# Optimization experiments

Measured on AMD Instinct MI355X. Metric: run time of the kernel, lower is better.

## Reference

```python
import jax, jax.numpy as jnp
import numpy as np

# static config (matches init_kwargs)
B, H, W, C = 8, 64, 64, 512
HEADS, WS, SHIFT = 16, 8, 4
N = WS * WS
HIDDEN = 4 * C
HEAD_DIM = C // HEADS
SCALE = HEAD_DIM ** -0.5
EPS = 1e-3  # keras LayerNormalization default epsilon


def _rel_pos_index(ws):
    # replicates tf.meshgrid default 'xy' indexing used in the source
    coords = np.stack(np.meshgrid(np.arange(ws), np.arange(ws)))  # [2, ws, ws]
    cf = coords.reshape(2, -1)
    rel = (cf[:, :, None] - cf[:, None, :]).transpose(1, 2, 0)  # [N, N, 2]
    rel[:, :, 0] += ws - 1
    rel[:, :, 1] += ws - 1
    rel[:, :, 0] *= 2 * ws - 1
    return jnp.asarray(rel.sum(-1))  # [N, N] int


def _attn_mask(h, w, ws, shift):
    img = np.zeros((h, w), dtype=np.float32)
    cnt = 0
    for hs in (slice(0, -ws), slice(-ws, -shift), slice(-shift, None)):
        for wsl in (slice(0, -ws), slice(-ws, -shift), slice(-shift, None)):
            img[hs, wsl] = cnt
            cnt += 1
    mw = img.reshape(h // ws, ws, w // ws, ws).transpose(0, 2, 1, 3).reshape(-1, ws * ws)  # [nW, N]
    diff = mw[:, None, :] - mw[:, :, None]
    return jnp.asarray(np.where(diff != 0, -100.0, 0.0).astype(np.float32))  # [nW, N, N]


REL_IDX = _rel_pos_index(WS)
ATTN_MASK = _attn_mask(H, W, WS, SHIFT)
NW = (H // WS) * (W // WS)


def _ln(x, g, b):
    mu = jnp.mean(x, -1, keepdims=True)
    var = jnp.mean(jnp.square(x - mu), -1, keepdims=True)
    return (x - mu) * jax.lax.rsqrt(var + EPS) * g + b


def setup_inputs() -> dict:
    key = jax.random.key(0)
    ks = jax.random.split(key, 14)
    s = 0.02
    return {
        "x": jax.random.normal(ks[0], (B, H * W, C), jnp.float32),
        "norm1_g": jnp.ones((C,), jnp.float32),
        "norm1_b": jnp.zeros((C,), jnp.float32),
        "qkv_w": jax.random.normal(ks[1], (C, 3 * C), jnp.float32) * s,
        "qkv_b": jnp.zeros((3 * C,), jnp.float32),
        "rpb_table": jax.random.normal(ks[2], ((2 * WS - 1) ** 2, HEADS), jnp.float32) * s,
        "proj_w": jax.random.normal(ks[3], (C, C), jnp.float32) * s,
        "proj_b": jnp.zeros((C,), jnp.float32),
        "norm2_g": jnp.ones((C,), jnp.float32),
        "norm2_b": jnp.zeros((C,), jnp.float32),
        "fc1_w": jax.random.normal(ks[4], (C, HIDDEN), jnp.float32) * s,
        "fc1_b": jnp.zeros((HIDDEN,), jnp.float32),
        "fc2_w": jax.random.normal(ks[5], (HIDDEN, C), jnp.float32) * s,
        "fc2_b": jnp.zeros((C,), jnp.float32),
    }


def reference(x, norm1_g, norm1_b, qkv_w, qkv_b, rpb_table, proj_w, proj_b,
              norm2_g, norm2_b, fc1_w, fc1_b, fc2_w, fc2_b):
    shortcut = x
    h = _ln(x, norm1_g, norm1_b).reshape(B, H, W, C)
    # cyclic shift (SW-MSA)
    h = jnp.roll(h, (-SHIFT, -SHIFT), axis=(1, 2))
    # window partition -> (B*nW, N, C)
    h = h.reshape(B, H // WS, WS, W // WS, WS, C).transpose(0, 1, 3, 2, 4, 5)
    h = h.reshape(B * NW, N, C)
    # qkv
    qkv = (h @ qkv_w + qkv_b).reshape(B * NW, N, 3, HEADS, HEAD_DIM).transpose(2, 0, 3, 1, 4)
    q, k, v = qkv[0] * SCALE, qkv[1], qkv[2]  # each [Bw, heads, N, hd]
    attn = jnp.einsum('bhnd,bhmd->bhnm', q, k)  # [Bw, heads, N, N]
    bias = rpb_table[REL_IDX.reshape(-1)].reshape(N, N, HEADS).transpose(2, 0, 1)
    attn = attn + bias[None]
    # shifted-window mask, per source: mask add -> softmax -> softmax AGAIN (source quirk)
    attn = attn.reshape(B, NW, HEADS, N, N) + ATTN_MASK[None, :, None]
    attn = attn.reshape(B * NW, HEADS, N, N)
    attn = jax.nn.softmax(attn, axis=-1)
    attn = jax.nn.softmax(attn, axis=-1)
    o = jnp.einsum('bhnm,bhmd->bhnd', attn, v).transpose(0, 2, 1, 3).reshape(B * NW, N, C)
    o = o @ proj_w + proj_b
    # window reverse + reverse shift
    o = o.reshape(B, H // WS, W // WS, WS, WS, C).transpose(0, 1, 3, 2, 4, 5).reshape(B, H, W, C)
    o = jnp.roll(o, (SHIFT, SHIFT), axis=(1, 2)).reshape(B, H * W, C)
    x = shortcut + o
    # MLP: source applies gelu twice (Dense activation + explicit gelu)
    y = _ln(x, norm2_g, norm2_b)
    y = jax.nn.gelu(jax.nn.gelu(y @ fc1_w + fc1_b, approximate=False), approximate=False)
    y = y @ fc2_w + fc2_b
    return x + y
```

## Files before the change

### kernel.cpp

```cpp
#include <hip/hip_runtime.h>
#include <hip/hip_bf16.h>
#include <math.h>


typedef unsigned short ushort_t;
typedef __attribute__((ext_vector_type(8))) short short8;
typedef __attribute__((ext_vector_type(8))) __bf16 bf16x8;
typedef __attribute__((ext_vector_type(4))) float f32x4;

#define DEVINL __device__ __forceinline__

union frag_u { short8 s; bf16x8 b; };

DEVINL float bf2f(ushort_t u){ union {unsigned int i; float f;} c; c.i = ((unsigned)u)<<16; return c.f; }
DEVINL ushort_t f2bf(float f){ union {unsigned int i; float f;} c; c.f = f; unsigned r = c.i + 0x7fffu + ((c.i>>16)&1u); return (ushort_t)(r>>16); }

typedef const __attribute__((address_space(1))) void* gas_t;
typedef __attribute__((address_space(3))) void* las_t;
DEVINL void load_lds16(const void* g, void* l) {
  __builtin_amdgcn_global_load_lds((gas_t)g, (las_t)l, 16, 0, 0);
}

DEVINL float gelu_fast(float v){
  float z  = fabsf(v) * 0.70710678118654752f;
  float t  = __builtin_amdgcn_rcpf(fmaf(0.47047f, z, 1.0f));
  float p  = t * fmaf(t, fmaf(t, 0.7478556f, -0.0958798f), 0.3480242f);
  float e  = __expf(-z*z);
  float er = fmaf(-p, e, 1.0f);
  float hs = (v >= 0.f) ? 0.5f : -0.5f;
  return v * fmaf(hs, er, 0.5f);
}

DEVINL int win_map_row(int t){
  int bw = t >> 6, n = t & 63;
  int b  = bw >> 6, wdx = bw & 63;
  int wh = wdx >> 3, ww = wdx & 7;
  int r  = n >> 3,  c  = n & 7;
  int hh = (wh*8 + r + 4) & 63;
  int w2 = (ww*8 + c + 4) & 63;
  return (b << 12) + (hh << 6) + w2;
}

__global__ void transpose_f2b(const float* __restrict__ in, ushort_t* __restrict__ out,
                              int R, int Ccols){
  __shared__ float t[32][33];
  int bx = blockIdx.x*32, by = blockIdx.y*32;
  int x = threadIdx.x, y = threadIdx.y;
  #pragma unroll
  for (int i=0;i<32;i+=8) t[y+i][x] = in[(size_t)(by+y+i)*Ccols + bx + x];
  __syncthreads();
  #pragma unroll
  for (int i=0;i<32;i+=8) out[(size_t)(bx+y+i)*R + by + x] = f2bf(t[x][y+i]);
}

__global__ __launch_bounds__(256) void ln_kernel(const float* __restrict__ in,
    const float* __restrict__ g, const float* __restrict__ bta,
    ushort_t* __restrict__ out, int windowed){
  int tid = threadIdx.x; int l = tid & 63; int w = tid >> 6;
  int t = blockIdx.x * 4 + w;
  int src = windowed ? win_map_row(t) : t;
  const float* row = in + (size_t)src * 512;
  float4 v0 = *(const float4*)(row + l*8);
  float4 v1 = *(const float4*)(row + l*8 + 4);
  float f[8] = {v0.x,v0.y,v0.z,v0.w, v1.x,v1.y,v1.z,v1.w};
  float s=0.f, s2=0.f;
  #pragma unroll
  for (int j=0;j<8;j++){ s += f[j]; s2 += f[j]*f[j]; }
  #pragma unroll
  for (int m=1;m<64;m<<=1){ s += __shfl_xor(s,m); s2 += __shfl_xor(s2,m); }
  float mu  = s * (1.f/512.f);
  float var = s2*(1.f/512.f) - mu*mu;
  float rs  = rsqrtf(var + 1e-3f);
  float4 g0 = *(const float4*)(g + l*8),   g1 = *(const float4*)(g + l*8 + 4);
  float4 b0 = *(const float4*)(bta + l*8), b1 = *(const float4*)(bta + l*8 + 4);
  float gg[8] = {g0.x,g0.y,g0.z,g0.w, g1.x,g1.y,g1.z,g1.w};
  float bb[8] = {b0.x,b0.y,b0.z,b0.w, b1.x,b1.y,b1.z,b1.w};
  short8 o;
  #pragma unroll
  for (int j=0;j<8;j++) o[j] = (short)f2bf((f[j]-mu)*rs*gg[j] + bb[j]);
  *(short8*)(out + (size_t)t*512 + l*8) = o;
}

#define G_STAGE(G, base, h, tt, LB) do { \
    load_lds16((G) + (base) + (size_t)((h)*128)*K    + (size_t)(tt)*64, &lds[(LB) + (h)*8192 +        w*512]); \
    load_lds16((G) + (base) + (size_t)((h)*128+64)*K + (size_t)(tt)*64, &lds[(LB) + (h)*8192 + 4096 + w*512]); \
  } while(0)

#define NOWAIT
#define VM4 asm volatile("s_waitcnt vmcnt(4)" ::: "memory")

#define PHASE(mp, STAGE_STMT, EXTRA) do { \
    bf16x8 a0 = *(const bf16x8*)&lds[ALb + aoff[2*(mp)  ][0]]; \
    bf16x8 a1 = *(const bf16x8*)&lds[ALb + aoff[2*(mp)  ][1]]; \
    bf16x8 a2 = *(const bf16x8*)&lds[ALb + aoff[2*(mp)+1][0]]; \
    bf16x8 a3 = *(const bf16x8*)&lds[ALb + aoff[2*(mp)+1][1]]; \
    STAGE_STMT; \
    EXTRA; \
    __builtin_amdgcn_s_barrier(); \
    asm volatile("s_waitcnt lgkmcnt(0)" ::: "memory"); \
    __builtin_amdgcn_sched_barrier(0); \
    __builtin_amdgcn_s_setprio(1); \
    _Pragma("unroll") \
    for (int nf=0; nf<4; nf++){ \
      acc[2*(mp)  ][nf] = __builtin_amdgcn_mfma_f32_16x16x32_bf16(a0, bfr[nf][0], acc[2*(mp)  ][nf], 0,0,0); \
      acc[2*(mp)  ][nf] = __builtin_amdgcn_mfma_f32_16x16x32_bf16(a1, bfr[nf][1], acc[2*(mp)  ][nf], 0,0,0); \
      acc[2*(mp)+1][nf] = __builtin_amdgcn_mfma_f32_16x16x32_bf16(a2, bfr[nf][0], acc[2*(mp)+1][nf], 0,0,0); \
      acc[2*(mp)+1][nf] = __builtin_amdgcn_mfma_f32_16x16x32_bf16(a3, bfr[nf][1], acc[2*(mp)+1][nf], 0,0,0); \
    } \
    __builtin_amdgcn_s_setprio(0); \
    __builtin_amdgcn_sched_barrier(0); \
    __builtin_amdgcn_s_barrier(); \
  } while(0)

template<int EPI>
__global__ __launch_bounds__(512, 2) void gemm256(
    const ushort_t* __restrict__ A, const ushort_t* __restrict__ Bt,
    const float* __restrict__ bias, void* __restrict__ Cout_v,
    const float* __restrict__ xres, int M, int N, int K)
{
  __shared__ ushort_t lds[65536];
  const int tid = threadIdx.x; const int l = tid & 63; const int w = tid >> 6;
  const int wm = w >> 2, wn = w & 3;
  const int m0 = blockIdx.x*256, n0 = blockIdx.y*256;
  const int lr = l & 15, lk = l >> 4;
  const int nt = K >> 6;

  const int r0 = tid >> 3;
  const int kc = ((tid & 7) - r0) & 7;
  const size_t aRow0 = (size_t)(m0 + r0) * K + kc * 8;
  const size_t bRow0 = (size_t)(n0 + r0) * K + kc * 8;

  int aoff[8][2], boff[4][2];
  #pragma unroll
  for (int mf=0; mf<8; mf++){
    int row = wm*128 + mf*16 + lr;
    #pragma unroll
    for (int kh=0; kh<2; kh++){ int c = kh*4 + lk; aoff[mf][kh] = (row*8 + ((c + row)&7))*8; }
  }
  #pragma unroll
  for (int nf=0; nf<4; nf++){
    int row = wn*64 + nf*16 + lr;
    #pragma unroll
    for (int kh=0; kh<2; kh++){ int c = kh*4 + lk; boff[nf][kh] = (row*8 + ((c + row)&7))*8; }
  }

  f32x4 acc[8][4] = {};

  G_STAGE(A,  aRow0, 0, 0, 0);
  G_STAGE(A,  aRow0, 1, 0, 0);
  G_STAGE(Bt, bRow0, 0, 0, 16384);
  G_STAGE(Bt, bRow0, 1, 0, 16384);
  G_STAGE(Bt, bRow0, 0, 1, 32768+16384);
  G_STAGE(Bt, bRow0, 1, 1, 32768+16384);
  VM4;
  __builtin_amdgcn_s_barrier();

  #pragma unroll 2
  for (int t = 0; t < nt; ++t) {
    const int b   = t & 1;
    const int ALb = b*32768, BLb = ALb + 16384;
    const int ALn = (b^1)*32768;
    const int t1  = (t+1 < nt) ? t+1 : t;
    const int t2  = (t+2 < nt) ? t+2 : t;

    bf16x8 bfr[4][2];
    #pragma unroll
    for (int nf=0; nf<4; nf++){
      bfr[nf][0] = *(const bf16x8*)&lds[BLb + boff[nf][0]];
      bfr[nf][1] = *(const bf16x8*)&lds[BLb + boff[nf][1]];
    }
    PHASE(0, G_STAGE(A,  aRow0, 0, t1, ALn), NOWAIT);
    PHASE(1, G_STAGE(A,  aRow0, 1, t1, ALn), NOWAIT);
    PHASE(2, G_STAGE(Bt, bRow0, 0, t2, BLb), NOWAIT);
    PHASE(3, G_STAGE(Bt, bRow0, 1, t2, BLb), VM4);
  }

  #pragma unroll
  for (int mf=0; mf<8; mf++){
    int rbase = m0 + wm*128 + mf*16 + lk*4;
    #pragma unroll
    for (int nf=0; nf<4; nf++){
      int col = n0 + wn*64 + nf*16 + lr;
      float bz = bias[col];
      #pragma unroll
      for (int rg=0; rg<4; rg++){
        int grow = rbase + rg;
        float v = acc[mf][nf][rg] + bz;
        if (EPI == 1){
          v = gelu_fast(gelu_fast(v));
        }
        if (EPI == 0 || EPI == 1){
          ((ushort_t*)Cout_v)[(size_t)grow*N + col] = f2bf(v);
        } else if (EPI == 2){
          int row2 = win_map_row(grow);
          size_t off = (size_t)row2*512 + col;
          ((float*)Cout_v)[off] = xres[off] + v;
        } else {
          size_t off = (size_t)grow*N + col;
          ((float*)Cout_v)[off] += v;
        }
      }
    }
  }
}

DEVINL int band3(int t){ return (t<56) ? 0 : ((t<60) ? 1 : 2); }

__global__ __launch_bounds__(256) void attn_kernel(const ushort_t* __restrict__ qkv,
    const float* __restrict__ rpb, ushort_t* __restrict__ o)
{
  __shared__ ushort_t sP[4][64*64];
  __shared__ ushort_t sV[4][64*32];
  int tid = threadIdx.x; int l = tid & 63; int w = tid >> 6;
  int p = blockIdx.x*4 + w;
  int bw = p >> 4, head = p & 15;
  int lr = l & 15, lk = l >> 4;
  const ushort_t* base = qkv + (size_t)bw*64*1536 + head*32;

  #pragma unroll
  for (int c=0;c<4;c++){
    int idx = c*64 + l;
    int row = idx >> 2, cc = idx & 3;
    load_lds16(base + 1024 + (size_t)row*1536 + cc*8, &sV[w][0] + c*512);
  }

  bf16x8 qf[4], kf[4];
  #pragma unroll
  for (int m=0;m<4;m++) qf[m] = *(const bf16x8*)(base +       (size_t)(m*16+lr)*1536 + lk*8);
  #pragma unroll
  for (int m=0;m<4;m++) kf[m] = *(const bf16x8*)(base + 512 + (size_t)(m*16+lr)*1536 + lk*8);

  f32x4 s[4][4] = {};
  #pragma unroll
  for (int m=0;m<4;m++)
    #pragma unroll
    for (int n=0;n<4;n++)
      s[m][n] = __builtin_amdgcn_mfma_f32_16x16x32_bf16(qf[m], kf[n], s[m][n], 0,0,0);

  int wdx = bw & 63; int wh = wdx >> 3, ww = wdx & 7;
  const float SCALE = 0.17677669529663687f;
  #pragma unroll
  for (int m=0;m<4;m++){
    #pragma unroll
    for (int r=0;r<4;r++){
      int i  = m*16 + lk*4 + r;
      int ri = band3(wh*8 + (i>>3))*3 + band3(ww*8 + (i&7));
      int ix = i & 7, iy = i >> 3;
      #pragma unroll
      for (int n=0;n<4;n++){
        int j   = n*16 + lr;
        int rj  = band3(wh*8 + (j>>3))*3 + band3(ww*8 + (j&7));
        int idx = 15*(ix - (j&7) + 7) + (iy - (j>>3) + 7);
        float bv = rpb[idx*16 + head];
        float mk = (ri == rj) ? 0.f : -100.f;
        s[m][n][r] = s[m][n][r]*SCALE + bv + mk;
      }
    }
  }

  #pragma unroll
  for (int pass=0; pass<2; pass++){
    #pragma unroll
    for (int m=0;m<4;m++){
      #pragma unroll
      for (int r=0;r<4;r++){
        float mx = fmaxf(fmaxf(s[m][0][r], s[m][1][r]), fmaxf(s[m][2][r], s[m][3][r]));
        #pragma unroll
        for (int d=1;d<16;d<<=1) mx = fmaxf(mx, __shfl_xor(mx, d));
        float sum = 0.f;
        #pragma unroll
        for (int n=0;n<4;n++){ float e = __expf(s[m][n][r]-mx); s[m][n][r]=e; sum += e; }
        #pragma unroll
        for (int d=1;d<16;d<<=1) sum += __shfl_xor(sum, d);
        float inv = 1.f/sum;
        #pragma unroll
        for (int n=0;n<4;n++) s[m][n][r] = s[m][n][r]*inv;
      }
    }
  }

  ushort_t* pl = &sP[w][0];
  #pragma unroll
  for (int m=0;m<4;m++)
    #pragma unroll
    for (int r=0;r<4;r++){
      int i = m*16 + lk*4 + r;
      #pragma unroll
      for (int n=0;n<4;n++){
        int j = n*16 + lr;
        int byte = i*128 + ((j*2) ^ ((i&7)<<4));
        pl[byte>>1] = f2bf(s[m][n][r]);
      }
    }

  asm volatile("s_waitcnt vmcnt(0)" ::: "memory");
  const ushort_t* vl = &sV[w][0];
  frag_u vf[2][2];
  #pragma unroll
  for (int kb=0;kb<2;kb++)
    #pragma unroll
    for (int nb=0;nb<2;nb++){
      #pragma unroll
      for (int j=0;j<8;j++){
        int k = kb*32 + lk*8 + j;
        vf[kb][nb].s[j] = (short)vl[k*32 + nb*16 + lr];
      }
    }

  f32x4 oacc[4][2] = {};
  #pragma unroll
  for (int m=0;m<4;m++){
    #pragma unroll
    for (int kb=0;kb<2;kb++){
      int row  = m*16 + lr;
      int byte = row*128 + ((kb*64 + lk*16) ^ ((row&7)<<4));
      bf16x8 pf = *(const bf16x8*)(pl + (byte>>1));
      #pragma unroll
      for (int nb=0;nb<2;nb++)
        oacc[m][nb] = __builtin_amdgcn_mfma_f32_16x16x32_bf16(pf, vf[kb][nb].b, oacc[m][nb], 0,0,0);
    }
  }

  ushort_t* orow = o + (size_t)bw*64*512 + head*32;
  #pragma unroll
  for (int m=0;m<4;m++)
    #pragma unroll
    for (int nb=0;nb<2;nb++)
      #pragma unroll
      for (int r=0;r<4;r++){
        int i = m*16 + lk*4 + r;
        int d = nb*16 + lr;
        orow[(size_t)i*512 + d] = f2bf(oacc[m][nb][r]);
      }
}

extern "C" void kernel_launch(void* const* d_in, const int* in_sizes, int n_in,
                              void* d_out, int out_size, void* d_ws, size_t ws_size,
                              hipStream_t stream) {
  const float* x      = (const float*)d_in[0];
  const float* n1g    = (const float*)d_in[1];
  const float* n1b    = (const float*)d_in[2];
  const float* qkv_w  = (const float*)d_in[3];
  const float* qkv_b  = (const float*)d_in[4];
  const float* rpb    = (const float*)d_in[5];
  const float* proj_w = (const float*)d_in[6];
  const float* proj_b = (const float*)d_in[7];
  const float* n2g    = (const float*)d_in[8];
  const float* n2b    = (const float*)d_in[9];
  const float* fc1_w  = (const float*)d_in[10];
  const float* fc1_b  = (const float*)d_in[11];
  const float* fc2_w  = (const float*)d_in[12];
  const float* fc2_b  = (const float*)d_in[13];
  float* out = (float*)d_out;

  ushort_t* ws = (ushort_t*)d_ws;
  size_t off = 0;
  ushort_t* wqT = ws + off; off += (size_t)1536*512;
  ushort_t* wpT = ws + off; off += (size_t)512*512;
  ushort_t* w1T = ws + off; off += (size_t)2048*512;
  ushort_t* w2T = ws + off; off += (size_t)512*2048;
  ushort_t* R1  = ws + off; off += (size_t)32768*512;
  ushort_t* R2  = ws + off; off += (size_t)32768*2048;
  if (ws_size < off*sizeof(ushort_t)) return;

  dim3 tb(32,8);
  transpose_f2b<<<dim3(48,16), tb, 0, stream>>>(qkv_w, wqT, 512, 1536);
  transpose_f2b<<<dim3(16,16), tb, 0, stream>>>(proj_w, wpT, 512, 512);
  transpose_f2b<<<dim3(64,16), tb, 0, stream>>>(fc1_w, w1T, 512, 2048);
  transpose_f2b<<<dim3(16,64), tb, 0, stream>>>(fc2_w, w2T, 2048, 512);

  ln_kernel<<<8192, 256, 0, stream>>>(x, n1g, n1b, R1, 1);
  gemm256<0><<<dim3(128, 6), 512, 0, stream>>>(R1, wqT, qkv_b, R2, nullptr, 32768, 1536, 512);
  attn_kernel<<<2048, 256, 0, stream>>>(R2, rpb, R1);
  gemm256<2><<<dim3(128, 2), 512, 0, stream>>>(R1, wpT, proj_b, out, x, 32768, 512, 512);
  ln_kernel<<<8192, 256, 0, stream>>>(out, n2g, n2b, R1, 0);
  gemm256<1><<<dim3(128, 8), 512, 0, stream>>>(R1, w1T, fc1_b, R2, nullptr, 32768, 2048, 512);
  gemm256<3><<<dim3(128, 2), 512, 0, stream>>>(R2, w2T, fc2_b, out, nullptr, 32768, 512, 2048);
}
```

Measured before the change: 457.6 us.

## Use simpler 128x128 single-buffered GEMM kernel for FC1 layer

Adds a new gemm_bt kernel with 128x128 tiles, 256 threads, K-step 32, swizzled LDS layout and direct global-to-LDS loads, and uses it for the FC1 GEMM with its double-GELU epilogue in place of the 256-tile double-buffered kernel. It also drops the unroll-2 pragma on the main loop of the existing gemm256 kernel. The smaller tiles give more blocks and the launch bounds allow two blocks per CU, aiming for better occupancy on the wide FC1 output. In exchange the new kernel has no software pipelining, syncs twice per K-step and reuses less data per tile.

```diff
diff --git a/kernel.cpp b/kernel.cpp
--- a/kernel.cpp
+++ b/kernel.cpp
@@ -79,6 +79,79 @@
   #pragma unroll
   for (int j=0;j<8;j++) o[j] = (short)f2bf((f[j]-mu)*rs*gg[j] + bb[j]);
   *(short8*)(out + (size_t)t*512 + l*8) = o;
+}
+
+template<int EPI>
+__global__ __launch_bounds__(256, 2) void gemm_bt(
+    const ushort_t* __restrict__ A, const ushort_t* __restrict__ Bt,
+    const float* __restrict__ bias, void* __restrict__ Cout_v,
+    const float* __restrict__ xres, int M, int N, int K)
+{
+  __shared__ ushort_t lA[128*32];
+  __shared__ ushort_t lB[128*32];
+  int tid = threadIdx.x; int l = tid & 63; int w = tid >> 6;
+  int m0 = blockIdx.x*128, n0 = blockIdx.y*128;
+  int wr = (w>>1)*64, wc = (w&1)*64;
+  int lr = l & 15, lk = l >> 4;
+
+  f32x4 acc[4][4] = {};
+  for (int k0 = 0; k0 < K; k0 += 32) {
+    #pragma unroll
+    for (int i=0;i<2;i++){
+      int s   = i*256 + tid;
+      int row = s >> 2;
+      int cg  = ((s&3) - (row>>1)) & 3;
+      ushort_t* ldst  = lA + (size_t)(i*256 + w*64)*8;
+      load_lds16(A  + (size_t)(m0+row)*K + (k0 + cg*8), ldst);
+      ushort_t* ldstB = lB + (size_t)(i*256 + w*64)*8;
+      load_lds16(Bt + (size_t)(n0+row)*K + (k0 + cg*8), ldstB);
+    }
+    __syncthreads();
+    bf16x8 af[4], bfr[4];
+    #pragma unroll
+    for (int m=0;m<4;m++){
+      int row  = wr + m*16 + lr;
+      int slot = row*4 + ((lk + (row>>1)) & 3);
+      af[m] = *(const bf16x8*)(lA + slot*8);
+    }
+    #pragma unroll
+    for (int n=0;n<4;n++){
+      int row  = wc + n*16 + lr;
+      int slot = row*4 + ((lk + (row>>1)) & 3);
+      bfr[n] = *(const bf16x8*)(lB + slot*8);
+    }
+    #pragma unroll
+    for (int m=0;m<4;m++)
+      #pragma unroll
+      for (int n=0;n<4;n++)
+        acc[m][n] = __builtin_amdgcn_mfma_f32_16x16x32_bf16(af[m], bfr[n], acc[m][n], 0,0,0);
+    __syncthreads();
+  }
+  #pragma unroll
+  for (int m=0;m<4;m++){
+    int rloc = wr + m*16 + lk*4;
+    #pragma unroll
+    for (int n=0;n<4;n++){
+      int col = n0 + wc + n*16 + lr;
+      float bz = bias[col];
+      #pragma unroll
+      for (int r=0;r<4;r++){
+        int grow = m0 + rloc + r;
+        float v = acc[m][n][r] + bz;
+        if (EPI == 1) v = gelu_fast(gelu_fast(v));
+        if (EPI == 0 || EPI == 1){
+          ((ushort_t*)Cout_v)[(size_t)grow*N + col] = f2bf(v);
+        } else if (EPI == 2){
+          int row2 = win_map_row(grow);
+          size_t off = (size_t)row2*512 + col;
+          ((float*)Cout_v)[off] = xres[off] + v;
+        } else {
+          size_t off = (size_t)grow*N + col;
+          ((float*)Cout_v)[off] += v;
+        }
+      }
+    }
+  }
 }
 
 #define G_STAGE(G, base, h, tt, LB) do { \
@@ -155,7 +228,6 @@
   VM4;
   __builtin_amdgcn_s_barrier();
 
-  #pragma unroll 2
   for (int t = 0; t < nt; ++t) {
     const int b   = t & 1;
     const int ALb = b*32768, BLb = ALb + 16384;
@@ -186,9 +258,7 @@
       for (int rg=0; rg<4; rg++){
         int grow = rbase + rg;
         float v = acc[mf][nf][rg] + bz;
-        if (EPI == 1){
-          v = gelu_fast(gelu_fast(v));
-        }
+        if (EPI == 1) v = gelu_fast(gelu_fast(v));
         if (EPI == 0 || EPI == 1){
           ((ushort_t*)Cout_v)[(size_t)grow*N + col] = f2bf(v);
         } else if (EPI == 2){
@@ -374,6 +444,6 @@
   attn_kernel<<<2048, 256, 0, stream>>>(R2, rpb, R1);
   gemm256<2><<<dim3(128, 2), 512, 0, stream>>>(R1, wpT, proj_b, out, x, 32768, 512, 512);
   ln_kernel<<<8192, 256, 0, stream>>>(out, n2g, n2b, R1, 0);
-  gemm256<1><<<dim3(128, 8), 512, 0, stream>>>(R1, w1T, fc1_b, R2, nullptr, 32768, 2048, 512);
+  gemm_bt<1><<<dim3(256, 16), 256, 0, stream>>>(R1, w1T, fc1_b, R2, nullptr, 32768, 2048, 512);
   gemm256<3><<<dim3(128, 2), 512, 0, stream>>>(R2, w2T, fc2_b, out, nullptr, 32768, 512, 2048);
 }
```

Result: faster. 445.9 us (-2.6%).
